# Optimization experiments

Hardware: AMD Instinct MI355X
Metric: run time of the kernel (lower is better)

## Reference

```python
import jax, jax.numpy as jnp
import numpy as np

D_MODEL = 384
N_HEADS = 8
HEAD_DIM = D_MODEL // N_HEADS


def setup_inputs() -> dict:
    key = jax.random.key(0)
    ks = jax.random.split(key, 8)
    b, n = 2, 2048
    s = 0.02
    return {
        "x": jax.random.normal(ks[0], (b, n, D_MODEL), jnp.float32),
        "coords": jax.random.normal(ks[1], (b, n, 3), jnp.float32),
        "W_qkv": jax.random.normal(ks[2], (D_MODEL, 3 * D_MODEL), jnp.float32) * s,
        "b_qkv": jnp.zeros((3 * D_MODEL,), jnp.float32),
        "W_dist": jax.random.normal(ks[3], (1, N_HEADS), jnp.float32) * s,
        "b_dist": jnp.zeros((N_HEADS,), jnp.float32),
        "W_out": jax.random.normal(ks[4], (D_MODEL, D_MODEL), jnp.float32) * s,
        "b_out": jnp.zeros((D_MODEL,), jnp.float32),
    }


def reference(x, coords, W_qkv, b_qkv, W_dist, b_dist, W_out, b_out):
    b, n, _ = x.shape
    qkv = x @ W_qkv + b_qkv                       # (b, n, 3*d)
    q, k, v = jnp.split(qkv, 3, axis=-1)
    def heads(t):
        return t.reshape(b, n, N_HEADS, HEAD_DIM).transpose(0, 2, 1, 3)  # b h n d
    q, k, v = heads(q), heads(k), heads(v)
    attn = jnp.einsum('bhid,bhjd->bhij', q, k) / jnp.sqrt(jnp.float32(HEAD_DIM))
    # distance bias: ||c_i - c_j|| projected to heads (Linear(1, n_heads))
    diff = coords[:, :, None, :] - coords[:, None, :, :]   # (b, i, j, 3)
    dist = jnp.sqrt(jnp.sum(diff * diff, axis=-1))         # (b, i, j)
    dist_bias = dist[..., None] * W_dist[0] + b_dist       # (b, i, j, h)
    attn = attn + dist_bias.transpose(0, 3, 1, 2)          # (b, h, i, j)
    attn = jax.nn.softmax(attn, axis=-1)
    out = jnp.einsum('bhij,bhjd->bhid', attn, v)
    out = out.transpose(0, 2, 1, 3).reshape(b, n, D_MODEL)
    return out @ W_out + b_out
```

## Files before the change

kernel.cpp:

```cpp
#include <hip/hip_runtime.h>
#include <hip/hip_bf16.h>

#define NB 2
#define SEQ 2048
#define DM 384
#define NH 8
#define HD 48
#define QKVN 1152

typedef __hip_bfloat16 bf16;
typedef __attribute__((ext_vector_type(8))) short short8;
typedef __attribute__((ext_vector_type(4))) float float4v;
typedef __attribute__((ext_vector_type(16))) float f32x16;

static __device__ __forceinline__ float bf2f(bf16 v){ return __bfloat162float(v); }
static __device__ __forceinline__ float ldin(const void* p, size_t i, int isf){
    return isf ? ((const float*)p)[i] : bf2f(((const bf16*)p)[i]);
}
static __device__ __forceinline__ short f2b(float f){
    union { float f; unsigned u; } a; a.f = f;
    unsigned r = a.u + 0x7FFFu + ((a.u >> 16) & 1u);
    return (short)(r >> 16);
}
static __device__ __forceinline__ unsigned pk2(float a, float b){
    union { __hip_bfloat162 h; unsigned u; } r;
    r.h = __float22bfloat162_rn(float2{a, b});
    return r.u;
}
static __device__ __forceinline__ short8 u4pack(unsigned w0, unsigned w1, unsigned w2, unsigned w3){
    union { unsigned u[4]; short8 s; } r; r.u[0]=w0; r.u[1]=w1; r.u[2]=w2; r.u[3]=w3; return r.s;
}
static __device__ __forceinline__ int detect_isf(const void* x){
    const unsigned short* xb = (const unsigned short*)x;
    int l = threadIdx.x & 63;
    union { unsigned u; float f; } a; a.u = ((unsigned)xb[2*l]) << 16;
    float ab = fabsf(a.f);
    int good = (a.f == 0.0f) || (ab > 9.765625e-4f && ab < 1024.0f);
    unsigned long long m = __ballot(good);
    return (__popcll(m) >= 32) ? 0 : 1;
}

__global__ __launch_bounds__(256) void k_prep(const void* __restrict__ x,
    const void* __restrict__ coords,
    const void* __restrict__ Wqkv, const void* __restrict__ Wout,
    const void* __restrict__ bqkv, const void* __restrict__ bout,
    const void* __restrict__ Wdist, const void* __restrict__ bdist,
    float* __restrict__ cjf, short* __restrict__ xb,
    short* __restrict__ WqT, short* __restrict__ WoT,
    float* __restrict__ bqf, float* __restrict__ bof,
    float* __restrict__ wdf, float* __restrict__ bdf)
{
    const int isf = detect_isf(x);
    const int t = threadIdx.x;
    const int b = blockIdx.x;
    if (b < 8) {
        #pragma unroll
        for (int k = 0; k < 2; ++k) {
            int e = b*512 + k*256 + t;
            int bb = e >> 11, jj = e & 2047;
            size_t gi = ((size_t)bb*SEQ + jj)*3;
            float4 cv;
            cv.x = ldin(coords, gi, isf);
            cv.y = ldin(coords, gi+1, isf);
            cv.z = ldin(coords, gi+2, isf);
            cv.w = 0.0f;
            ((float4*)cjf)[e] = cv;
        }
    } else if (b < 776) {
        size_t i = ((size_t)(b-8)*256 + t)*8;
        if (isf) {
            const float* xf = (const float*)x + i;
            short o[8];
            #pragma unroll
            for (int e = 0; e < 8; ++e) o[e] = f2b(xf[e]);
            *(int4*)(xb + i) = *(const int4*)o;
        } else {
            *(int4*)(xb + i) = *(const int4*)((const short*)x + i);
        }
    } else if (b < 1352) {
        int bb, NW; const void* W; short* WT;
        if (b < 1208) { bb = b - 776;  NW = QKVN; W = Wqkv; WT = WqT; }
        else          { bb = b - 1208; NW = DM;   W = Wout; WT = WoT; }
        int ntiles = NW >> 5;
        int kt = bb / ntiles, nt = bb % ntiles;
        int k0 = kt*32, n0 = nt*32;
        __shared__ float Ls[32][33];
        for (int idx = t; idx < 1024; idx += 256) {
            int r = idx >> 5, c = idx & 31;
            Ls[r][c] = ldin(W, (size_t)(k0+r)*NW + n0 + c, isf);
        }
        __syncthreads();
        for (int idx = t; idx < 1024; idx += 256) {
            int r2 = idx >> 5, c2 = idx & 31;
            WT[(size_t)(n0+r2)*DM + k0 + c2] = f2b(Ls[c2][r2]);
        }
    } else {
        int idx = (b - 1352)*256 + t;
        const float log2e = 1.4426950408889634f;
        if (idx < QKVN) bqf[idx] = ldin(bqkv, idx, isf);
        else if (idx < QKVN + DM) bof[idx - QKVN] = ldin(bout, idx - QKVN, isf);
        else if (idx < QKVN + DM + NH) wdf[idx - QKVN - DM] = ldin(Wdist, idx - QKVN - DM, isf)*log2e;
        else if (idx < QKVN + DM + 2*NH) bdf[idx - QKVN - DM - NH] = ldin(bdist, idx - QKVN - DM - NH, isf)*log2e;
    }
}

__global__ __launch_bounds__(256) void k_qkv(const short* __restrict__ xb,
    const short* __restrict__ WT, const float* __restrict__ bias,
    short* __restrict__ qg3, short* __restrict__ kg3, short* __restrict__ vg3)
{
    __shared__ __align__(16) short As[64*72];
    __shared__ __align__(16) short Bs[128*72];
    const int t = threadIdx.x;
    const int w = t >> 6, lane = t & 63, L = lane & 15, quad = lane >> 4;
    const int mt = blockIdx.x / 9, nt = blockIdx.x % 9;
    const int row0 = mt*64, col0 = nt*128;
    const int wm = w & 1, wn = w >> 1;
    float4v acc[2][4] = {};
    for (int k0 = 0; k0 < DM; k0 += 64) {
        __syncthreads();
        for (int c = t; c < 512; c += 256) {
            int row = c >> 3, k8 = c & 7;
            *(int4*)(&As[row*72 + k8*8]) = *(const int4*)(xb + (size_t)(row0+row)*DM + k0 + k8*8);
        }
        for (int c = t; c < 1024; c += 256) {
            int row = c >> 3, k8 = c & 7;
            *(int4*)(&Bs[row*72 + k8*8]) = *(const int4*)(WT + (size_t)(col0+row)*DM + k0 + k8*8);
        }
        __syncthreads();
        #pragma unroll
        for (int kc = 0; kc < 2; ++kc) {
            short8 a0 = *(const short8*)(&As[(32*wm + L)*72 + kc*32 + quad*8]);
            short8 a1 = *(const short8*)(&As[(32*wm + 16 + L)*72 + kc*32 + quad*8]);
            #pragma unroll
            for (int ni = 0; ni < 4; ++ni) {
                short8 bf = *(const short8*)(&Bs[(64*wn + 16*ni + L)*72 + kc*32 + quad*8]);
                acc[0][ni] = __builtin_amdgcn_mfma_f32_16x16x32_bf16(a0, bf, acc[0][ni], 0, 0, 0);
                acc[1][ni] = __builtin_amdgcn_mfma_f32_16x16x32_bf16(a1, bf, acc[1][ni], 0, 0, 0);
            }
        }
    }
    const int which = col0 / DM;
    const int cbase = col0 % DM;
    short* Ep = Bs;
    __syncthreads();
    if (which < 2) {
        #pragma unroll
        for (int mi = 0; mi < 2; ++mi)
            #pragma unroll
            for (int ni = 0; ni < 4; ++ni) {
                int col_l = 64*wn + 16*ni + L;
                float bv = bias[col0 + col_l];
                #pragma unroll
                for (int r = 0; r < 4; ++r) {
                    int row_l = 32*wm + 16*mi + quad*4 + r;
                    Ep[row_l*136 + col_l] = f2b(acc[mi][ni][r] + bv);
                }
            }
        __syncthreads();
        short* dst = which ? kg3 : qg3;
        for (int c = t; c < 1024; c += 256) {
            int row_l = c >> 4, col_l = (c & 15)*8;
            int row_g = row0 + row_l;
            int bi = row_g >> 11, nn = row_g & (SEQ-1);
            int c2 = cbase + col_l;
            int hh = c2/HD, dh = c2%HD;
            int bh = bi*NH + hh;
            int dc = dh >> 4, hi = (dh >> 3) & 1;
            size_t dstoff = ((size_t)bh*64 + (nn>>5))*1536 + (size_t)((dc*2 + hi)*256 + (nn&31)*8);
            *(int4*)(dst + dstoff) = *(const int4*)(&Ep[row_l*136 + col_l]);
        }
    } else {
        #pragma unroll
        for (int mi = 0; mi < 2; ++mi)
            #pragma unroll
            for (int ni = 0; ni < 4; ++ni) {
                int col_l = 64*wn + 16*ni + L;
                float bv = bias[col0 + col_l];
                #pragma unroll
                for (int r = 0; r < 4; ++r) {
                    int row_l = 32*wm + 16*mi + quad*4 + r;
                    Ep[col_l*72 + row_l] = f2b(acc[mi][ni][r] + bv);
                }
            }
        __syncthreads();
        for (int c = t; c < 1024; c += 256) {
            int col_l = c >> 3, row8 = (c & 7)*8;
            int row_g = row0 + row8;
            int bi = row_g >> 11, nn = row_g & (SEQ-1);
            int c2 = cbase + col_l;
            int hh = c2/HD, dh = c2%HD;
            int bh = bi*NH + hh;
            int jt = nn >> 5, jc = (nn >> 4) & 1;
            int ehalf = ((nn >> 3) & 1)*4;
            int dt = dh >> 5, dp = dh & 31;
            int hstride = dt ? 128 : 256;
            size_t base = ((size_t)bh*64 + jt)*1536 + (size_t)(jc*768 + dt*512 + dp*8 + ehalf);
            *(int2*)(vg3 + base)           = *(const int2*)(&Ep[col_l*72 + row8]);
            *(int2*)(vg3 + base + hstride) = *(const int2*)(&Ep[col_l*72 + row8 + 4]);
        }
    }
}

__global__ __launch_bounds__(256, 2) void k_attn(
    const short* __restrict__ qg3, const short* __restrict__ kg3, const short* __restrict__ vg3,
    const float* __restrict__ cjf, const float* __restrict__ wdf,
    const float* __restrict__ bdf, short* __restrict__ aob)
{
    __shared__ float4 cjs[2048];
    __shared__ float Ored[2][64*48];
    __shared__ float Lred[2][64];
    const int t = threadIdx.x;
    const int w = t >> 6, lane = t & 63;
    const int li = lane & 31, hi = lane >> 5;
    const int lg = (blockIdx.x & 7)*64 + (blockIdx.x >> 3);
    const int bh = lg >> 5, it = lg & 31;
    const int bi = bh >> 3, hh = bh & 7;
    const int i0 = it*64;
    const float scale2 = 0.14433756729740643f * 1.4426950408889634f;
    const float wd = wdf[hh], bd = bdf[hh];

    for (int c = t; c < 2048; c += 256)
        cjs[c] = ((const float4*)cjf)[(size_t)bi*2048 + c];
    float cix[2], ciy[2], ciz[2];
    #pragma unroll
    for (int m = 0; m < 2; ++m) {
        float4 cv = ((const float4*)cjf)[(size_t)bi*2048 + i0 + m*32 + li];
        cix[m] = cv.x; ciy[m] = cv.y; ciz[m] = cv.z;
    }
    const short* qB = qg3 + ((size_t)bh*64 + it*2)*1536 + hi*256 + li*8;
    short8 qf[2][3];
    #pragma unroll
    for (int m = 0; m < 2; ++m)
        #pragma unroll
        for (int d = 0; d < 3; ++d)
            qf[m][d] = *(const short8*)(qB + m*1536 + d*512);
    __syncthreads();

    f32x16 aO0[2] = {}, aO1[2] = {};
    float rsum[2] = {};

    const short* kBp = kg3 + ((size_t)bh*64 + w)*1536 + hi*256 + li*8;
    const short* vBp = vg3 + ((size_t)bh*64 + w)*1536 + li*8;
    int jb = w*32 + hi*4;

    for (int s = 0; s < 16; ++s) {
        short8 kf0 = *(const short8*)(kBp);
        short8 kf1 = *(const short8*)(kBp + 512);
        short8 kf2 = *(const short8*)(kBp + 1024);
        short8 v00 = *(const short8*)(vBp + hi*256);
        short8 v10 = *(const short8*)(vBp + 768 + hi*256);
        short8 v01 = *(const short8*)(vBp + 512 + hi*128);
        short8 v11 = *(const short8*)(vBp + 1280 + hi*128);
        f32x16 s0 = {}, s1 = {};
        s0 = __builtin_amdgcn_mfma_f32_32x32x16_bf16(kf0, qf[0][0], s0, 0, 0, 0);
        s1 = __builtin_amdgcn_mfma_f32_32x32x16_bf16(kf0, qf[1][0], s1, 0, 0, 0);
        s0 = __builtin_amdgcn_mfma_f32_32x32x16_bf16(kf1, qf[0][1], s0, 0, 0, 0);
        s1 = __builtin_amdgcn_mfma_f32_32x32x16_bf16(kf1, qf[1][1], s1, 0, 0, 0);
        s0 = __builtin_amdgcn_mfma_f32_32x32x16_bf16(kf2, qf[0][2], s0, 0, 0, 0);
        s1 = __builtin_amdgcn_mfma_f32_32x32x16_bf16(kf2, qf[1][2], s1, 0, 0, 0);
        unsigned pw0[8], pw1[8];
        #pragma unroll
        for (int rq = 0; rq < 4; ++rq) {
            float p0[4], p1[4];
            #pragma unroll
            for (int q = 0; q < 4; ++q) {
                float4 cj = cjs[jb + 8*rq + q];
                int r = 4*rq + q;
                float dx0 = cix[0]-cj.x, dy0 = ciy[0]-cj.y, dz0 = ciz[0]-cj.z;
                float dd0 = sqrtf(dx0*dx0 + dy0*dy0 + dz0*dz0);
                float dx1 = cix[1]-cj.x, dy1 = ciy[1]-cj.y, dz1 = ciz[1]-cj.z;
                float dd1 = sqrtf(dx1*dx1 + dy1*dy1 + dz1*dz1);
                p0[q] = __builtin_amdgcn_exp2f(fmaf(s0[r], scale2, fmaf(dd0, wd, bd)));
                p1[q] = __builtin_amdgcn_exp2f(fmaf(s1[r], scale2, fmaf(dd1, wd, bd)));
            }
            rsum[0] += (p0[0] + p0[1]) + (p0[2] + p0[3]);
            rsum[1] += (p1[0] + p1[1]) + (p1[2] + p1[3]);
            pw0[2*rq]   = pk2(p0[0], p0[1]);
            pw0[2*rq+1] = pk2(p0[2], p0[3]);
            pw1[2*rq]   = pk2(p1[0], p1[1]);
            pw1[2*rq+1] = pk2(p1[2], p1[3]);
        }
        short8 pa00 = u4pack(pw0[0], pw0[1], pw0[2], pw0[3]);
        short8 pa01 = u4pack(pw0[4], pw0[5], pw0[6], pw0[7]);
        short8 pa10 = u4pack(pw1[0], pw1[1], pw1[2], pw1[3]);
        short8 pa11 = u4pack(pw1[4], pw1[5], pw1[6], pw1[7]);
        aO0[0] = __builtin_amdgcn_mfma_f32_32x32x16_bf16(pa00, v00, aO0[0], 0, 0, 0);
        aO0[0] = __builtin_amdgcn_mfma_f32_32x32x16_bf16(pa01, v10, aO0[0], 0, 0, 0);
        aO1[0] = __builtin_amdgcn_mfma_f32_32x32x16_bf16(pa00, v01, aO1[0], 0, 0, 0);
        aO1[0] = __builtin_amdgcn_mfma_f32_32x32x16_bf16(pa01, v11, aO1[0], 0, 0, 0);
        aO0[1] = __builtin_amdgcn_mfma_f32_32x32x16_bf16(pa10, v00, aO0[1], 0, 0, 0);
        aO0[1] = __builtin_amdgcn_mfma_f32_32x32x16_bf16(pa11, v10, aO0[1], 0, 0, 0);
        aO1[1] = __builtin_amdgcn_mfma_f32_32x32x16_bf16(pa10, v01, aO1[1], 0, 0, 0);
        aO1[1] = __builtin_amdgcn_mfma_f32_32x32x16_bf16(pa11, v11, aO1[1], 0, 0, 0);
        kBp += 4*1536; vBp += 4*1536; jb += 128;
    }
    #pragma unroll
    for (int m = 0; m < 2; ++m)
        rsum[m] += __shfl_xor(rsum[m], 32);

    if (w >= 2) {
        float* Od = Ored[w-2];
        #pragma unroll
        for (int m = 0; m < 2; ++m)
            #pragma unroll
            for (int r = 0; r < 16; ++r) {
                int ii = m*32 + (r & 3) + 8*(r >> 2) + 4*hi;
                Od[ii*48 + li] = aO0[m][r];
                if (li < 16) Od[ii*48 + 32 + li] = aO1[m][r];
            }
        if (lane < 32) { Lred[w-2][li] = rsum[0]; Lred[w-2][32 + li] = rsum[1]; }
    }
    __syncthreads();
    if (w < 2) {
        const float* Od = Ored[w];
        #pragma unroll
        for (int m = 0; m < 2; ++m)
            #pragma unroll
            for (int r = 0; r < 16; ++r) {
                int ii = m*32 + (r & 3) + 8*(r >> 2) + 4*hi;
                aO0[m][r] += Od[ii*48 + li];
                aO1[m][r] += Od[ii*48 + 32 + (li & 15)];
            }
        rsum[0] += Lred[w][li]; rsum[1] += Lred[w][32 + li];
    }
    __syncthreads();
    if (w == 1) {
        float* Od = Ored[0];
        #pragma unroll
        for (int m = 0; m < 2; ++m)
            #pragma unroll
            for (int r = 0; r < 16; ++r) {
                int ii = m*32 + (r & 3) + 8*(r >> 2) + 4*hi;
                Od[ii*48 + li] = aO0[m][r];
                if (li < 16) Od[ii*48 + 32 + li] = aO1[m][r];
            }
        if (lane < 32) { Lred[0][li] = rsum[0]; Lred[0][32 + li] = rsum[1]; }
    }
    __syncthreads();
    if (w == 0) {
        float* Od = Ored[0];
        #pragma unroll
        for (int m = 0; m < 2; ++m)
            #pragma unroll
            for (int r = 0; r < 16; ++r) {
                int ii = m*32 + (r & 3) + 8*(r >> 2) + 4*hi;
                Od[ii*48 + li] += aO0[m][r];
                if (li < 16) Od[ii*48 + 32 + li] += aO1[m][r];
            }
        if (lane < 32) { Lred[0][li] += rsum[0]; Lred[0][32 + li] += rsum[1]; }
    }
    __syncthreads();
    for (int c = t; c < 384; c += 256) {
        int r = c / 6, d8 = (c % 6)*8;
        float inv = 1.0f / Lred[0][r];
        const float* src = &Ored[0][r*48 + d8];
        short o[8];
        #pragma unroll
        for (int e = 0; e < 8; ++e) o[e] = f2b(src[e]*inv);
        *(int4*)(aob + ((size_t)(bi*SEQ) + i0 + r)*DM + hh*HD + d8) = *(const int4*)o;
    }
}

__global__ __launch_bounds__(256) void k_out(const short* __restrict__ aob,
    const short* __restrict__ WT, const float* __restrict__ bias,
    void* __restrict__ out, const void* __restrict__ x)
{
    __shared__ __align__(16) short As[64*72];
    __shared__ __align__(16) short Bs[128*72];
    const int isf = detect_isf(x);
    const int t = threadIdx.x;
    const int w = t >> 6, lane = t & 63, L = lane & 15, quad = lane >> 4;
    const int mt = blockIdx.x / 3, nt = blockIdx.x % 3;
    const int row0 = mt*64, col0 = nt*128;
    const int wm = w & 1, wn = w >> 1;
    float4v acc[2][4] = {};
    for (int k0 = 0; k0 < DM; k0 += 64) {
        __syncthreads();
        for (int c = t; c < 512; c += 256) {
            int row = c >> 3, k8 = c & 7;
            *(int4*)(&As[row*72 + k8*8]) = *(const int4*)(aob + (size_t)(row0+row)*DM + k0 + k8*8);
        }
        for (int c = t; c < 1024; c += 256) {
            int row = c >> 3, k8 = c & 7;
            *(int4*)(&Bs[row*72 + k8*8]) = *(const int4*)(WT + (size_t)(col0+row)*DM + k0 + k8*8);
        }
        __syncthreads();
        #pragma unroll
        for (int kc = 0; kc < 2; ++kc) {
            short8 a0 = *(const short8*)(&As[(32*wm + L)*72 + kc*32 + quad*8]);
            short8 a1 = *(const short8*)(&As[(32*wm + 16 + L)*72 + kc*32 + quad*8]);
            #pragma unroll
            for (int ni = 0; ni < 4; ++ni) {
                short8 bf = *(const short8*)(&Bs[(64*wn + 16*ni + L)*72 + kc*32 + quad*8]);
                acc[0][ni] = __builtin_amdgcn_mfma_f32_16x16x32_bf16(a0, bf, acc[0][ni], 0, 0, 0);
                acc[1][ni] = __builtin_amdgcn_mfma_f32_16x16x32_bf16(a1, bf, acc[1][ni], 0, 0, 0);
            }
        }
    }
    #pragma unroll
    for (int mi = 0; mi < 2; ++mi) {
        #pragma unroll
        for (int ni = 0; ni < 4; ++ni) {
            int col_g = col0 + 64*wn + 16*ni + L;
            float bv = bias[col_g];
            #pragma unroll
            for (int r = 0; r < 4; ++r) {
                int row_g = row0 + 32*wm + 16*mi + quad*4 + r;
                size_t oi = (size_t)row_g*DM + col_g;
                float val = acc[mi][ni][r] + bv;
                if (isf) ((float*)out)[oi] = val;
                else     ((bf16*)out)[oi]  = __float2bfloat16(val);
            }
        }
    }
}

extern "C" void kernel_launch(void* const* d_in, const int* in_sizes, int n_in,
                              void* d_out, int out_size, void* d_ws, size_t ws_size,
                              hipStream_t stream) {
    const void* x      = d_in[0];
    const void* coords = d_in[1];
    const void* Wqkv   = d_in[2];
    const void* bqkv   = d_in[3];
    const void* Wdist  = d_in[4];
    const void* bdist  = d_in[5];
    const void* Wout   = d_in[6];
    const void* bout   = d_in[7];

    short* qg3   = (short*)d_ws;
    short* kg3   = qg3  + (size_t)1572864;
    short* vg3   = kg3  + (size_t)1572864;
    short* aob   = vg3  + (size_t)1573120;
    short* xb    = aob  + (size_t)1572864;
    short* WqT   = xb   + (size_t)1572864;
    short* WoT   = WqT  + (size_t)442368;
    float* bqf   = (float*)(WoT + (size_t)147456);
    float* bof   = bqf + QKVN;
    float* wdf   = bof + DM;
    float* bdf   = wdf + NH;
    float* cjf   = bdf + NH;

    k_prep<<<dim3(1359), dim3(256), 0, stream>>>(x, coords, Wqkv, Wout, bqkv, bout,
                                                 Wdist, bdist, cjf, xb, WqT, WoT,
                                                 bqf, bof, wdf, bdf);
    k_qkv<<<dim3(64*9), dim3(256), 0, stream>>>(xb, WqT, bqf, qg3, kg3, vg3);
    k_attn<<<dim3(512), dim3(256), 0, stream>>>(qg3, kg3, vg3, cjf, wdf, bdf, aob);
    k_out<<<dim3(64*3), dim3(256), 0, stream>>>(aob, WoT, bof, d_out, x);
}
```

Baseline: 174.2 us.

## Precompute pairwise distance matrix in bf16 and fuse x conversion into QKV GEMM

```diff
diff --git a/kernel.cpp b/kernel.cpp
--- a/kernel.cpp
+++ b/kernel.cpp
@@ -26,6 +26,12 @@
     union { __hip_bfloat162 h; unsigned u; } r;
     r.h = __float22bfloat162_rn(float2{a, b});
     return r.u;
+}
+static __device__ __forceinline__ float bflo(unsigned u){
+    union { unsigned u; float f; } a; a.u = u << 16; return a.f;
+}
+static __device__ __forceinline__ float bfhi(unsigned u){
+    union { unsigned u; float f; } a; a.u = u & 0xFFFF0000u; return a.f;
 }
 static __device__ __forceinline__ short8 u4pack(unsigned w0, unsigned w1, unsigned w2, unsigned w3){
     union { unsigned u[4]; short8 s; } r; r.u[0]=w0; r.u[1]=w1; r.u[2]=w2; r.u[3]=w3; return r.s;
@@ -45,7 +51,7 @@
     const void* __restrict__ Wqkv, const void* __restrict__ Wout,
     const void* __restrict__ bqkv, const void* __restrict__ bout,
     const void* __restrict__ Wdist, const void* __restrict__ bdist,
-    float* __restrict__ cjf, short* __restrict__ xb,
+    short* __restrict__ dist8,
     short* __restrict__ WqT, short* __restrict__ WoT,
     float* __restrict__ bqf, float* __restrict__ bof,
     float* __restrict__ wdf, float* __restrict__ bdf)
@@ -53,34 +59,40 @@
     const int isf = detect_isf(x);
     const int t = threadIdx.x;
     const int b = blockIdx.x;
-    if (b < 8) {
-        #pragma unroll
-        for (int k = 0; k < 2; ++k) {
-            int e = b*512 + k*256 + t;
-            int bb = e >> 11, jj = e & 2047;
-            size_t gi = ((size_t)bb*SEQ + jj)*3;
-            float4 cv;
-            cv.x = ldin(coords, gi, isf);
-            cv.y = ldin(coords, gi+1, isf);
-            cv.z = ldin(coords, gi+2, isf);
-            cv.w = 0.0f;
-            ((float4*)cjf)[e] = cv;
-        }
-    } else if (b < 776) {
-        size_t i = ((size_t)(b-8)*256 + t)*8;
-        if (isf) {
-            const float* xf = (const float*)x + i;
-            short o[8];
-            #pragma unroll
-            for (int e = 0; e < 8; ++e) o[e] = f2b(xf[e]);
-            *(int4*)(xb + i) = *(const int4*)o;
-        } else {
-            *(int4*)(xb + i) = *(const int4*)((const short*)x + i);
-        }
-    } else if (b < 1352) {
+    if (b < 512) {
+        const int bb = b >> 8;
+        const int jg = (b >> 1) & 127;
+        const int j0 = jg * 16;
+        const int ih = (b & 1) * 1024;
+        __shared__ float cjx[16], cjy[16], cjz[16];
+        if (t < 16) {
+            int gj = (bb*SEQ + j0 + t)*3;
+            cjx[t] = ldin(coords, gj, isf);
+            cjy[t] = ldin(coords, gj+1, isf);
+            cjz[t] = ldin(coords, gj+2, isf);
+        }
+        __syncthreads();
+        #pragma unroll
+        for (int k = 0; k < 4; ++k) {
+            int i = ih + k*256 + t;
+            int gi = (bb*SEQ + i)*3;
+            float px = ldin(coords, gi, isf), py = ldin(coords, gi+1, isf), pz = ldin(coords, gi+2, isf);
+            short o[16];
+            #pragma unroll
+            for (int e = 0; e < 16; ++e) {
+                float dx = px - cjx[e], dy = py - cjy[e], dz = pz - cjz[e];
+                o[e] = f2b(sqrtf(dx*dx + dy*dy + dz*dz));
+            }
+            short* dst = dist8 + (((size_t)bb*512 + (size_t)jg*4)*SEQ + i)*4;
+            *(int2*)(dst)          = *(const int2*)(o);
+            *(int2*)(dst + SEQ*4)  = *(const int2*)(o + 4);
+            *(int2*)(dst + SEQ*8)  = *(const int2*)(o + 8);
+            *(int2*)(dst + SEQ*12) = *(const int2*)(o + 12);
+        }
+    } else if (b < 1088) {
         int bb, NW; const void* W; short* WT;
-        if (b < 1208) { bb = b - 776;  NW = QKVN; W = Wqkv; WT = WqT; }
-        else          { bb = b - 1208; NW = DM;   W = Wout; WT = WoT; }
+        if (b < 944) { bb = b - 512; NW = QKVN; W = Wqkv; WT = WqT; }
+        else         { bb = b - 944; NW = DM;   W = Wout; WT = WoT; }
         int ntiles = NW >> 5;
         int kt = bb / ntiles, nt = bb % ntiles;
         int k0 = kt*32, n0 = nt*32;
@@ -95,7 +107,7 @@
             WT[(size_t)(n0+r2)*DM + k0 + c2] = f2b(Ls[c2][r2]);
         }
     } else {
-        int idx = (b - 1352)*256 + t;
+        int idx = (b - 1088)*256 + t;
         const float log2e = 1.4426950408889634f;
         if (idx < QKVN) bqf[idx] = ldin(bqkv, idx, isf);
         else if (idx < QKVN + DM) bof[idx - QKVN] = ldin(bout, idx - QKVN, isf);
@@ -104,12 +116,13 @@
     }
 }
 
-__global__ __launch_bounds__(256) void k_qkv(const short* __restrict__ xb,
+__global__ __launch_bounds__(256) void k_qkv(const void* __restrict__ x,
     const short* __restrict__ WT, const float* __restrict__ bias,
     short* __restrict__ qg3, short* __restrict__ kg3, short* __restrict__ vg3)
 {
     __shared__ __align__(16) short As[64*72];
     __shared__ __align__(16) short Bs[128*72];
+    const int isf = detect_isf(x);
     const int t = threadIdx.x;
     const int w = t >> 6, lane = t & 63, L = lane & 15, quad = lane >> 4;
     const int mt = blockIdx.x / 9, nt = blockIdx.x % 9;
@@ -120,7 +133,16 @@
         __syncthreads();
         for (int c = t; c < 512; c += 256) {
             int row = c >> 3, k8 = c & 7;
-            *(int4*)(&As[row*72 + k8*8]) = *(const int4*)(xb + (size_t)(row0+row)*DM + k0 + k8*8);
+            size_t src = (size_t)(row0+row)*DM + k0 + k8*8;
+            if (isf) {
+                const float* xf = (const float*)x + src;
+                short o[8];
+                #pragma unroll
+                for (int e = 0; e < 8; ++e) o[e] = f2b(xf[e]);
+                *(int4*)(&As[row*72 + k8*8]) = *(const int4*)o;
+            } else {
+                *(int4*)(&As[row*72 + k8*8]) = *(const int4*)((const short*)x + src);
+            }
         }
         for (int c = t; c < 1024; c += 256) {
             int row = c >> 3, k8 = c & 7;
@@ -203,10 +225,9 @@
 
 __global__ __launch_bounds__(256, 2) void k_attn(
     const short* __restrict__ qg3, const short* __restrict__ kg3, const short* __restrict__ vg3,
-    const float* __restrict__ cjf, const float* __restrict__ wdf,
+    const short* __restrict__ dist8, const float* __restrict__ wdf,
     const float* __restrict__ bdf, short* __restrict__ aob)
 {
-    __shared__ float4 cjs[2048];
     __shared__ float Ored[2][64*48];
     __shared__ float Lred[2][64];
     const int t = threadIdx.x;
@@ -219,14 +240,6 @@
     const float scale2 = 0.14433756729740643f * 1.4426950408889634f;
     const float wd = wdf[hh], bd = bdf[hh];
 
-    for (int c = t; c < 2048; c += 256)
-        cjs[c] = ((const float4*)cjf)[(size_t)bi*2048 + c];
-    float cix[2], ciy[2], ciz[2];
-    #pragma unroll
-    for (int m = 0; m < 2; ++m) {
-        float4 cv = ((const float4*)cjf)[(size_t)bi*2048 + i0 + m*32 + li];
-        cix[m] = cv.x; ciy[m] = cv.y; ciz[m] = cv.z;
-    }
     const short* qB = qg3 + ((size_t)bh*64 + it*2)*1536 + hi*256 + li*8;
     short8 qf[2][3];
     #pragma unroll
@@ -234,14 +247,13 @@
         #pragma unroll
         for (int d = 0; d < 3; ++d)
             qf[m][d] = *(const short8*)(qB + m*1536 + d*512);
-    __syncthreads();
 
     f32x16 aO0[2] = {}, aO1[2] = {};
     float rsum[2] = {};
 
     const short* kBp = kg3 + ((size_t)bh*64 + w)*1536 + hi*256 + li*8;
     const short* vBp = vg3 + ((size_t)bh*64 + w)*1536 + li*8;
-    int jb = w*32 + hi*4;
+    const short* dBp = dist8 + (((size_t)bi*512 + (size_t)w*8 + hi)*SEQ + i0 + li)*4;
 
     for (int s = 0; s < 16; ++s) {
         short8 kf0 = *(const short8*)(kBp);
@@ -261,18 +273,21 @@
         unsigned pw0[8], pw1[8];
         #pragma unroll
         for (int rq = 0; rq < 4; ++rq) {
+            int2 du0 = *(const int2*)(dBp + (size_t)SEQ*8*rq);
+            int2 du1 = *(const int2*)(dBp + 128 + (size_t)SEQ*8*rq);
             float p0[4], p1[4];
-            #pragma unroll
-            for (int q = 0; q < 4; ++q) {
-                float4 cj = cjs[jb + 8*rq + q];
-                int r = 4*rq + q;
-                float dx0 = cix[0]-cj.x, dy0 = ciy[0]-cj.y, dz0 = ciz[0]-cj.z;
-                float dd0 = sqrtf(dx0*dx0 + dy0*dy0 + dz0*dz0);
-                float dx1 = cix[1]-cj.x, dy1 = ciy[1]-cj.y, dz1 = ciz[1]-cj.z;
-                float dd1 = sqrtf(dx1*dx1 + dy1*dy1 + dz1*dz1);
-                p0[q] = __builtin_amdgcn_exp2f(fmaf(s0[r], scale2, fmaf(dd0, wd, bd)));
-                p1[q] = __builtin_amdgcn_exp2f(fmaf(s1[r], scale2, fmaf(dd1, wd, bd)));
-            }
+            float a0 = bflo((unsigned)du0.x), a1 = bfhi((unsigned)du0.x);
+            float a2 = bflo((unsigned)du0.y), a3 = bfhi((unsigned)du0.y);
+            float b0 = bflo((unsigned)du1.x), b1 = bfhi((unsigned)du1.x);
+            float b2 = bflo((unsigned)du1.y), b3 = bfhi((unsigned)du1.y);
+            p0[0] = __builtin_amdgcn_exp2f(fmaf(s0[4*rq+0], scale2, fmaf(a0, wd, bd)));
+            p0[1] = __builtin_amdgcn_exp2f(fmaf(s0[4*rq+1], scale2, fmaf(a1, wd, bd)));
+            p0[2] = __builtin_amdgcn_exp2f(fmaf(s0[4*rq+2], scale2, fmaf(a2, wd, bd)));
+            p0[3] = __builtin_amdgcn_exp2f(fmaf(s0[4*rq+3], scale2, fmaf(a3, wd, bd)));
+            p1[0] = __builtin_amdgcn_exp2f(fmaf(s1[4*rq+0], scale2, fmaf(b0, wd, bd)));
+            p1[1] = __builtin_amdgcn_exp2f(fmaf(s1[4*rq+1], scale2, fmaf(b1, wd, bd)));
+            p1[2] = __builtin_amdgcn_exp2f(fmaf(s1[4*rq+2], scale2, fmaf(b2, wd, bd)));
+            p1[3] = __builtin_amdgcn_exp2f(fmaf(s1[4*rq+3], scale2, fmaf(b3, wd, bd)));
             rsum[0] += (p0[0] + p0[1]) + (p0[2] + p0[3]);
             rsum[1] += (p1[0] + p1[1]) + (p1[2] + p1[3]);
             pw0[2*rq]   = pk2(p0[0], p0[1]);
@@ -292,7 +307,7 @@
         aO0[1] = __builtin_amdgcn_mfma_f32_32x32x16_bf16(pa11, v10, aO0[1], 0, 0, 0);
         aO1[1] = __builtin_amdgcn_mfma_f32_32x32x16_bf16(pa10, v01, aO1[1], 0, 0, 0);
         aO1[1] = __builtin_amdgcn_mfma_f32_32x32x16_bf16(pa11, v11, aO1[1], 0, 0, 0);
-        kBp += 4*1536; vBp += 4*1536; jb += 128;
+        kBp += 4*1536; vBp += 4*1536; dBp += (size_t)SEQ*128;
     }
     #pragma unroll
     for (int m = 0; m < 2; ++m)
@@ -430,20 +445,19 @@
     short* qg3   = (short*)d_ws;
     short* kg3   = qg3  + (size_t)1572864;
     short* vg3   = kg3  + (size_t)1572864;
-    short* aob   = vg3  + (size_t)1573120;
-    short* xb    = aob  + (size_t)1572864;
-    short* WqT   = xb   + (size_t)1572864;
+    short* dist8 = vg3  + (size_t)1573120;
+    short* aob   = dist8 + (size_t)8388608;
+    short* WqT   = aob  + (size_t)1572864;
     short* WoT   = WqT  + (size_t)442368;
     float* bqf   = (float*)(WoT + (size_t)147456);
     float* bof   = bqf + QKVN;
     float* wdf   = bof + DM;
     float* bdf   = wdf + NH;
-    float* cjf   = bdf + NH;
-
-    k_prep<<<dim3(1359), dim3(256), 0, stream>>>(x, coords, Wqkv, Wout, bqkv, bout,
-                                                 Wdist, bdist, cjf, xb, WqT, WoT,
+
+    k_prep<<<dim3(1095), dim3(256), 0, stream>>>(x, coords, Wqkv, Wout, bqkv, bout,
+                                                 Wdist, bdist, dist8, WqT, WoT,
                                                  bqf, bof, wdf, bdf);
-    k_qkv<<<dim3(64*9), dim3(256), 0, stream>>>(xb, WqT, bqf, qg3, kg3, vg3);
-    k_attn<<<dim3(512), dim3(256), 0, stream>>>(qg3, kg3, vg3, cjf, wdf, bdf, aob);
+    k_qkv<<<dim3(64*9), dim3(256), 0, stream>>>(x, WqT, bqf, qg3, kg3, vg3);
+    k_attn<<<dim3(512), dim3(256), 0, stream>>>(qg3, kg3, vg3, dist8, wdf, bdf, aob);
     k_out<<<dim3(64*3), dim3(256), 0, stream>>>(aob, WoT, bof, d_out, x);
 }
```

Result: faster. 162.2 us (-6.9%).
